# Optimization experiments

Hardware: AMD Instinct MI355X
Metric: run time of the kernel (lower is better)

## Reference

```python
import jax, jax.numpy as jnp
import numpy as np

B, S, D, H = 2, 2048, 1024, 16
HD = D // H  # head_dim = 64
SCALE = 1.0 / np.sqrt(np.float32(D))  # original divides by sqrt(d_keys) == sqrt(d_model)


def setup_inputs() -> dict:
    key = jax.random.key(0)
    ks = jax.random.split(key, 8)
    inp = {
        "query": jax.random.normal(ks[0], (B, S, D), jnp.float32),
        "key": jax.random.normal(ks[1], (B, S, D), jnp.float32),
        "value": jax.random.normal(ks[2], (B, S, D), jnp.float32),
        # nn.Linear weights stored as [out, in]; y = x @ W.T
        "Wq": jax.random.normal(ks[3], (D, D), jnp.float32) * 0.02,
        "Wk": jax.random.normal(ks[4], (D, D), jnp.float32) * 0.02,
        "Wv": jax.random.normal(ks[5], (D, D), jnp.float32) * 0.02,
        "Wo": jax.random.normal(ks[6], (D, D), jnp.float32) * 0.02,
        "bo": jax.random.normal(ks[7], (D,), jnp.float32) * 0.02,
    }
    return inp


def reference(query, key, value, Wq, Wk, Wv, Wo, bo):
    # projections (no bias)
    Q = jnp.einsum('bsd,ed->bse', query, Wq)
    K = jnp.einsum('bsd,ed->bse', key, Wk)
    V = jnp.einsum('bsd,ed->bse', value, Wv)
    # split heads -> [B, H, S, HD]
    Q = Q.reshape(B, S, H, HD).transpose(0, 2, 1, 3)
    K = K.reshape(B, S, H, HD).transpose(0, 2, 1, 3)
    V = V.reshape(B, S, H, HD).transpose(0, 2, 1, 3)
    # scores [B,H,S,S]; note: scaled by 1/sqrt(d_model), matching the source
    scores = jnp.einsum('bhqd,bhkd->bhqk', Q, K) * SCALE
    attn = jax.nn.softmax(scores, axis=-1)  # dropout_ratio=0 -> identity
    ctx = jnp.einsum('bhqk,bhkd->bhqd', attn, V)
    ctx = ctx.transpose(0, 2, 1, 3).reshape(B, S, D)
    return jnp.einsum('bsd,ed->bse', ctx, Wo) + bo
```

## Files before the change

kernel.cpp:

```cpp
#include <hip/hip_runtime.h>
#include <hip/hip_bf16.h>

#define B_  2
#define S_  2048
#define D_  1024
#define H_  16
#define HD_ 64
#define SCALE_ 0.03125f

typedef __bf16 bf16;
typedef __attribute__((ext_vector_type(8))) __bf16 bf16x8;
typedef __attribute__((ext_vector_type(8))) unsigned short u16x8;
typedef __attribute__((ext_vector_type(4))) __bf16 bf16x4;
typedef __attribute__((ext_vector_type(4))) float f32x4;

__device__ __forceinline__ void gload_lds16(const void* g, void* l) {
  __builtin_amdgcn_global_load_lds(
      (const __attribute__((address_space(1))) unsigned int*)g,
      (__attribute__((address_space(3))) unsigned int*)l,
      16, 0, 0);
}

__device__ __forceinline__ bf16x8 load8(const float* p) {
  const float4 a = *(const float4*)p;
  const float4 b = *(const float4*)(p + 4);
  bf16x8 r;
  r[0] = (bf16)a.x; r[1] = (bf16)a.y; r[2] = (bf16)a.z; r[3] = (bf16)a.w;
  r[4] = (bf16)b.x; r[5] = (bf16)b.y; r[6] = (bf16)b.z; r[7] = (bf16)b.w;
  return r;
}
__device__ __forceinline__ bf16x8 load8(const bf16* p) {
  return *(const bf16x8*)p;
}

__global__ __launch_bounds__(256)
void wconv_kernel(const float* __restrict__ Wq, const float* __restrict__ Wk,
                  const float* __restrict__ Wv, const float* __restrict__ Wo,
                  bf16* __restrict__ dst)
{
  const int n4  = (blockIdx.x * 256 + threadIdx.x) * 4;
  const int m   = n4 >> 20;
  const int off = n4 & ((1 << 20) - 1);
  const float* src = m == 0 ? Wq : (m == 1 ? Wk : (m == 2 ? Wv : Wo));
  const float4 a = *(const float4*)(src + off);
  bf16x4 o = {(bf16)a.x, (bf16)a.y, (bf16)a.z, (bf16)a.w};
  *(bf16x4*)(dst + n4) = o;
}

__global__ __launch_bounds__(256, 2)
void gemm_qkv_b_kernel(const float* __restrict__ Aq, const float* __restrict__ Ak,
                       const float* __restrict__ Av, const bf16* __restrict__ Wb,
                       bf16* __restrict__ Cq, bf16* __restrict__ Ck,
                       bf16* __restrict__ Cv)
{
  __shared__ bf16 lA[128 * 32];
  __shared__ bf16 lB[128 * 32];

  const int sel = blockIdx.y >> 3;
  const int bn  = blockIdx.y & 7;
  const float* A  = sel == 0 ? Aq : (sel == 1 ? Ak : Av);
  const bf16*  Bw = Wb + ((size_t)sel << 20);
  bf16*        C  = sel == 0 ? Cq : (sel == 1 ? Ck : Cv);
  const float scale = sel == 0 ? SCALE_ : 1.0f;

  const int t    = threadIdx.x;
  const int wave = t >> 6;
  const int lane = t & 63;
  const int quad = lane >> 4;
  const int l16  = lane & 15;
  const int bm = blockIdx.x;
  const int wm = (wave >> 1) * 64;
  const int wn = (wave & 1) * 64;

  const int srow = t >> 2;
  const int scol = (t & 3) * 8;
  const float* gA  = A  + (size_t)(bm * 128 + srow) * D_ + scol;
  const bf16*  gBb = Bw + (size_t)(bn * 128 + srow) * D_ + scol;

  f32x4 acc[4][4] = {};

  for (int k0 = 0; k0 < D_; k0 += 32) {
    const bf16x8 a0 = load8(gA);
    const bf16x8 a1 = load8(gA + (size_t)64 * D_);

    __syncthreads();
    *(bf16x8*)(lA + srow * 32 + scol)        = a0;
    *(bf16x8*)(lA + (srow + 64) * 32 + scol) = a1;
    gload_lds16(gBb,                   (char*)lB + wave * 1024);
    gload_lds16(gBb + (size_t)64 * D_, (char*)lB + 4096 + wave * 1024);
    __syncthreads();

    bf16x8 af[4], bfr[4];
#pragma unroll
    for (int i = 0; i < 4; ++i) {
      af[i]  = *(const bf16x8*)(lA + (wm + i * 16 + l16) * 32 + quad * 8);
      bfr[i] = *(const bf16x8*)(lB + (wn + i * 16 + l16) * 32 + quad * 8);
    }
#pragma unroll
    for (int mi = 0; mi < 4; ++mi)
#pragma unroll
      for (int ni = 0; ni < 4; ++ni)
        acc[mi][ni] = __builtin_amdgcn_mfma_f32_16x16x32_bf16(
            af[mi], bfr[ni], acc[mi][ni], 0, 0, 0);

    gA  += 32;
    gBb += 32;
  }

#pragma unroll
  for (int mi = 0; mi < 4; ++mi) {
#pragma unroll
    for (int ni = 0; ni < 4; ++ni) {
      const int col = bn * 128 + wn + ni * 16 + l16;
#pragma unroll
      for (int r = 0; r < 4; ++r) {
        const int row = bm * 128 + wm + mi * 16 + quad * 4 + r;
        C[(size_t)row * D_ + col] = (bf16)(acc[mi][ni][r] * scale);
      }
    }
  }
}

__global__ __launch_bounds__(256, 2)
void gemm_out_b_kernel(const bf16* __restrict__ A, const bf16* __restrict__ Bw,
                       const float* __restrict__ bias, float* __restrict__ C)
{
  __shared__ bf16 lA[128 * 32];
  __shared__ bf16 lB[64 * 32];

  const int t    = threadIdx.x;
  const int wave = t >> 6;
  const int lane = t & 63;
  const int quad = lane >> 4;
  const int l16  = lane & 15;
  const int bm = blockIdx.x;
  const int bn = blockIdx.y;
  const int wm = wave * 32;

  const int srow = t >> 2;
  const int scol = (t & 3) * 8;
  const bf16* gA = A  + (size_t)(bm * 128 + srow) * D_ + scol;
  const bf16* gB = Bw + (size_t)(bn * 64 + srow) * D_ + scol;

  f32x4 acc[2][4] = {};

  for (int k0 = 0; k0 < D_; k0 += 32) {
    __syncthreads();
    gload_lds16(gA,                   (char*)lA + wave * 1024);
    gload_lds16(gA + (size_t)64 * D_, (char*)lA + 4096 + wave * 1024);
    gload_lds16(gB,                   (char*)lB + wave * 1024);
    __syncthreads();

    bf16x8 af[2], bfr[4];
#pragma unroll
    for (int i = 0; i < 2; ++i)
      af[i]  = *(const bf16x8*)(lA + (wm + i * 16 + l16) * 32 + quad * 8);
#pragma unroll
    for (int i = 0; i < 4; ++i)
      bfr[i] = *(const bf16x8*)(lB + (i * 16 + l16) * 32 + quad * 8);
#pragma unroll
    for (int mi = 0; mi < 2; ++mi)
#pragma unroll
      for (int ni = 0; ni < 4; ++ni)
        acc[mi][ni] = __builtin_amdgcn_mfma_f32_16x16x32_bf16(
            af[mi], bfr[ni], acc[mi][ni], 0, 0, 0);

    gA += 32;
    gB += 32;
  }

  float bv[4];
#pragma unroll
  for (int ni = 0; ni < 4; ++ni)
    bv[ni] = bias[bn * 64 + ni * 16 + l16];
#pragma unroll
  for (int mi = 0; mi < 2; ++mi) {
#pragma unroll
    for (int ni = 0; ni < 4; ++ni) {
      const int col = bn * 64 + ni * 16 + l16;
#pragma unroll
      for (int r = 0; r < 4; ++r) {
        const int row = bm * 128 + wm + mi * 16 + quad * 4 + r;
        C[(size_t)row * D_ + col] = acc[mi][ni][r] + bv[ni];
      }
    }
  }
}

__global__ __launch_bounds__(256, 2)
void gemm_qkv_kernel(const float* __restrict__ Aq, const float* __restrict__ Ak,
                     const float* __restrict__ Av, const float* __restrict__ Wq,
                     const float* __restrict__ Wk, const float* __restrict__ Wv,
                     bf16* __restrict__ Cq, bf16* __restrict__ Ck,
                     bf16* __restrict__ Cv)
{
  __shared__ bf16 lA[128 * 32];
  __shared__ bf16 lB[128 * 32];

  const int sel = blockIdx.y >> 3;
  const int bn  = blockIdx.y & 7;
  const float* A  = sel == 0 ? Aq : (sel == 1 ? Ak : Av);
  const float* Bw = sel == 0 ? Wq : (sel == 1 ? Wk : Wv);
  bf16*        C  = sel == 0 ? Cq : (sel == 1 ? Ck : Cv);
  const float scale = sel == 0 ? SCALE_ : 1.0f;

  const int t    = threadIdx.x;
  const int wave = t >> 6;
  const int lane = t & 63;
  const int quad = lane >> 4;
  const int l16  = lane & 15;
  const int bm = blockIdx.x;
  const int wm = (wave >> 1) * 64;
  const int wn = (wave & 1) * 64;

  const int srow = t >> 2;
  const int scol = (t & 3) * 8;
  const float* gA = A  + (size_t)(bm * 128 + srow) * D_ + scol;
  const float* gB = Bw + (size_t)(bn * 128 + srow) * D_ + scol;

  f32x4 acc[4][4] = {};

  for (int k0 = 0; k0 < D_; k0 += 32) {
    const bf16x8 a0 = load8(gA);
    const bf16x8 a1 = load8(gA + (size_t)64 * D_);
    const bf16x8 b0 = load8(gB);
    const bf16x8 b1 = load8(gB + (size_t)64 * D_);

    __syncthreads();
    *(bf16x8*)(lA + srow * 32 + scol)        = a0;
    *(bf16x8*)(lA + (srow + 64) * 32 + scol) = a1;
    *(bf16x8*)(lB + srow * 32 + scol)        = b0;
    *(bf16x8*)(lB + (srow + 64) * 32 + scol) = b1;
    __syncthreads();

    bf16x8 af[4], bfr[4];
#pragma unroll
    for (int i = 0; i < 4; ++i) {
      af[i]  = *(const bf16x8*)(lA + (wm + i * 16 + l16) * 32 + quad * 8);
      bfr[i] = *(const bf16x8*)(lB + (wn + i * 16 + l16) * 32 + quad * 8);
    }
#pragma unroll
    for (int mi = 0; mi < 4; ++mi)
#pragma unroll
      for (int ni = 0; ni < 4; ++ni)
        acc[mi][ni] = __builtin_amdgcn_mfma_f32_16x16x32_bf16(
            af[mi], bfr[ni], acc[mi][ni], 0, 0, 0);

    gA += 32;
    gB += 32;
  }

#pragma unroll
  for (int mi = 0; mi < 4; ++mi) {
#pragma unroll
    for (int ni = 0; ni < 4; ++ni) {
      const int col = bn * 128 + wn + ni * 16 + l16;
#pragma unroll
      for (int r = 0; r < 4; ++r) {
        const int row = bm * 128 + wm + mi * 16 + quad * 4 + r;
        C[(size_t)row * D_ + col] = (bf16)(acc[mi][ni][r] * scale);
      }
    }
  }
}

__global__ __launch_bounds__(256, 2)
void gemm_out_kernel(const bf16* __restrict__ A, const float* __restrict__ Bw,
                     const float* __restrict__ bias, float* __restrict__ C)
{
  __shared__ bf16 lA[128 * 32];
  __shared__ bf16 lB[64 * 32];

  const int t    = threadIdx.x;
  const int wave = t >> 6;
  const int lane = t & 63;
  const int quad = lane >> 4;
  const int l16  = lane & 15;
  const int bm = blockIdx.x;
  const int bn = blockIdx.y;
  const int wm = wave * 32;

  const int srow = t >> 2;
  const int scol = (t & 3) * 8;
  const bf16*  gA = A  + (size_t)(bm * 128 + srow) * D_ + scol;
  const float* gB = Bw + (size_t)(bn * 64 + srow) * D_ + scol;

  f32x4 acc[2][4] = {};

  for (int k0 = 0; k0 < D_; k0 += 32) {
    const bf16x8 a0 = load8(gA);
    const bf16x8 a1 = load8(gA + (size_t)64 * D_);
    const bf16x8 b0 = load8(gB);

    __syncthreads();
    *(bf16x8*)(lA + srow * 32 + scol)        = a0;
    *(bf16x8*)(lA + (srow + 64) * 32 + scol) = a1;
    *(bf16x8*)(lB + srow * 32 + scol)        = b0;
    __syncthreads();

    bf16x8 af[2], bfr[4];
#pragma unroll
    for (int i = 0; i < 2; ++i)
      af[i]  = *(const bf16x8*)(lA + (wm + i * 16 + l16) * 32 + quad * 8);
#pragma unroll
    for (int i = 0; i < 4; ++i)
      bfr[i] = *(const bf16x8*)(lB + (i * 16 + l16) * 32 + quad * 8);
#pragma unroll
    for (int mi = 0; mi < 2; ++mi)
#pragma unroll
      for (int ni = 0; ni < 4; ++ni)
        acc[mi][ni] = __builtin_amdgcn_mfma_f32_16x16x32_bf16(
            af[mi], bfr[ni], acc[mi][ni], 0, 0, 0);

    gA += 32;
    gB += 32;
  }

  float bv[4];
#pragma unroll
  for (int ni = 0; ni < 4; ++ni)
    bv[ni] = bias[bn * 64 + ni * 16 + l16];
#pragma unroll
  for (int mi = 0; mi < 2; ++mi) {
#pragma unroll
    for (int ni = 0; ni < 4; ++ni) {
      const int col = bn * 64 + ni * 16 + l16;
#pragma unroll
      for (int r = 0; r < 4; ++r) {
        const int row = bm * 128 + wm + mi * 16 + quad * 4 + r;
        C[(size_t)row * D_ + col] = acc[mi][ni][r] + bv[ni];
      }
    }
  }
}

__global__ __launch_bounds__(256, 2)
void attn_kernel(const bf16* Q, const bf16* __restrict__ K,
                 const bf16* __restrict__ V, bf16* O)
{
  __shared__ bf16 lQ[64 * 72];
  __shared__ bf16 lK[64 * 72];
  __shared__ bf16 lVT[80 * 72];
  __shared__ bf16 lP[4][16 * 72];

  const int t    = threadIdx.x;
  const int wave = t >> 6;
  const int lane = t & 63;
  const int quad = lane >> 4;
  const int l16  = lane & 15;

  const int flat = blockIdx.y * 32 + blockIdx.x;
  const int qt   = (flat >> 3) & 31;
  const int bh   = (flat & 7) * 4 + (flat >> 8);
  const size_t headoff =
      (size_t)(bh >> 4) * ((size_t)S_ * D_) + (size_t)(bh & 15) * HD_;

  for (int i = t; i < 16 * 72; i += 256) {
    const int rr = i / 72, cc = i % 72;
    lVT[(64 + rr) * 72 + cc] = (bf16)((rr == 0 && cc < 64) ? 1.0f : 0.0f);
  }

  const int sr  = t >> 3;
  const int scx = (t & 7) * 8;
  {
    const bf16x8 q0 = *(const bf16x8*)(Q + headoff + (size_t)(qt * 64 + sr) * D_ + scx);
    const bf16x8 q1 = *(const bf16x8*)(Q + headoff + (size_t)(qt * 64 + sr + 32) * D_ + scx);
    *(bf16x8*)(lQ + sr * 72 + scx)        = q0;
    *(bf16x8*)(lQ + (sr + 32) * 72 + scx) = q1;
  }
  __syncthreads();

  bf16x8 qf[2];
  {
    const int row = wave * 16 + l16;
#pragma unroll
    for (int ks = 0; ks < 2; ++ks)
      qf[ks] = *(const bf16x8*)(lQ + row * 72 + (ks * 4 + quad) * 8);
  }

  f32x4 acco[4] = {};
  f32x4 acc4 = {};

  const int dp = t & 31;
  const int kg = t >> 5;

  bf16x8 pk0, pk1;
  unsigned int pv[8];
  {
    const bf16* kb = K + headoff + (size_t)(sr) * D_ + scx;
    pk0 = load8(kb);
    pk1 = load8(kb + (size_t)32 * D_);
    const bf16* vb = V + headoff + (size_t)(kg * 8) * D_ + 2 * dp;
#pragma unroll
    for (int j = 0; j < 8; ++j)
      pv[j] = *(const unsigned int*)(vb + (size_t)j * D_);
  }

  for (int kt = 0; kt < S_ / 64; ++kt) {
    __syncthreads();

    *(bf16x8*)(lK + sr * 72 + scx)        = pk0;
    *(bf16x8*)(lK + (sr + 32) * 72 + scx) = pk1;
    {
      u16x8 w0, w1;
#pragma unroll
      for (int j = 0; j < 8; ++j) {
        w0[j] = (unsigned short)(pv[j] & 0xffffu);
        w1[j] = (unsigned short)(pv[j] >> 16);
      }
      *(u16x8*)(lVT + (2 * dp) * 72 + kg * 8)     = w0;
      *(u16x8*)(lVT + (2 * dp + 1) * 72 + kg * 8) = w1;
    }
    __syncthreads();

    if (kt + 1 < S_ / 64) {
      const bf16* kb = K + headoff + (size_t)((kt + 1) * 64 + sr) * D_ + scx;
      pk0 = load8(kb);
      pk1 = load8(kb + (size_t)32 * D_);
      const bf16* vb = V + headoff + (size_t)((kt + 1) * 64 + kg * 8) * D_ + 2 * dp;
#pragma unroll
      for (int j = 0; j < 8; ++j)
        pv[j] = *(const unsigned int*)(vb + (size_t)j * D_);
    }

    f32x4 sc[4] = {};
#pragma unroll
    for (int nt = 0; nt < 4; ++nt) {
#pragma unroll
      for (int ks = 0; ks < 2; ++ks) {
        const int krow = nt * 16 + l16;
        const bf16x8 kf = *(const bf16x8*)(lK + krow * 72 + (ks * 4 + quad) * 8);
        sc[nt] = __builtin_amdgcn_mfma_f32_16x16x32_bf16(qf[ks], kf, sc[nt], 0, 0, 0);
      }
    }

    bf16* lPw = lP[wave];
#pragma unroll
    for (int nt = 0; nt < 4; ++nt) {
#pragma unroll
      for (int r = 0; r < 4; ++r) {
        const float p = __expf(sc[nt][r]);
        lPw[(quad * 4 + r) * 72 + nt * 16 + l16] = (bf16)p;
      }
    }

    bf16x8 pf[2];
#pragma unroll
    for (int ks = 0; ks < 2; ++ks)
      pf[ks] = *(const bf16x8*)(lPw + l16 * 72 + ks * 32 + quad * 8);
#pragma unroll
    for (int dt = 0; dt < 4; ++dt) {
#pragma unroll
      for (int ks = 0; ks < 2; ++ks) {
        const bf16x8 vf =
            *(const bf16x8*)(lVT + (dt * 16 + l16) * 72 + ks * 32 + quad * 8);
        acco[dt] = __builtin_amdgcn_mfma_f32_16x16x32_bf16(pf[ks], vf, acco[dt], 0, 0, 0);
      }
    }
#pragma unroll
    for (int ks = 0; ks < 2; ++ks) {
      const bf16x8 vf1 =
          *(const bf16x8*)(lVT + (64 + l16) * 72 + ks * 32 + quad * 8);
      acc4 = __builtin_amdgcn_mfma_f32_16x16x32_bf16(pf[ks], vf1, acc4, 0, 0, 0);
    }
  }

  float den[4];
#pragma unroll
  for (int r = 0; r < 4; ++r)
    den[r] = 1.f / __shfl(acc4[r], lane & 48);
#pragma unroll
  for (int dt = 0; dt < 4; ++dt) {
#pragma unroll
    for (int r = 0; r < 4; ++r) {
      const int row = qt * 64 + wave * 16 + quad * 4 + r;
      const int d   = dt * 16 + l16;
      O[headoff + (size_t)row * D_ + d] = (bf16)(acco[dt][r] * den[r]);
    }
  }
}

extern "C" void kernel_launch(void* const* d_in, const int* in_sizes, int n_in,
                              void* d_out, int out_size, void* d_ws, size_t ws_size,
                              hipStream_t stream)
{
  const float* q  = (const float*)d_in[0];
  const float* k  = (const float*)d_in[1];
  const float* v  = (const float*)d_in[2];
  const float* Wq = (const float*)d_in[3];
  const float* Wk = (const float*)d_in[4];
  const float* Wv = (const float*)d_in[5];
  const float* Wo = (const float*)d_in[6];
  const float* bo = (const float*)d_in[7];
  float* outf = (float*)d_out;
  bf16*  outs = (bf16*)d_out;
  bf16*  wsb  = (bf16*)d_ws;

  const size_t SD = (size_t)S_ * D_;
  const size_t MD = (size_t)B_ * S_ * D_;

  dim3 blk(256);
  dim3 gqkv(B_ * S_ / 128, 24);
  dim3 gattn(S_ / 64, B_ * H_);
  dim3 gout(B_ * S_ / 128, D_ / 64);

  bf16* Kp = outs;
  bf16* Vp = outs + MD;

  if (ws_size >= (size_t)16 << 20) {
    bf16* Wb = wsb;
    bf16* Qp = wsb + MD;

    wconv_kernel<<<4096, blk, 0, stream>>>(Wq, Wk, Wv, Wo, Wb);
    gemm_qkv_b_kernel<<<gqkv, blk, 0, stream>>>(q, k, v, Wb, Qp, Kp, Vp);
    attn_kernel<<<gattn, blk, 0, stream>>>(Qp, Kp, Vp, Qp);
    gemm_out_b_kernel<<<gout, blk, 0, stream>>>(Qp, Wb + 3 * ((size_t)1 << 20),
                                                bo, outf);
  } else {
    bf16* Qp = wsb;

    gemm_qkv_kernel<<<gqkv, blk, 0, stream>>>(q, k, v, Wq, Wk, Wv,
                                              Qp, Kp, Vp);
    attn_kernel<<<gattn, blk, 0, stream>>>(Qp, Kp, Vp, Qp);
    gemm_out_kernel<<<gout, blk, 0, stream>>>(Qp, Wo, bo, outf);
  }
}
```

Baseline: 234.8 us.

## Double attention query tile per block and fold log2e into Q scaling

Each attention block now processes 128 query rows instead of 64, with every wave handling two 16-row tiles. Each K and V fragment read from LDS therefore feeds two MFMAs, and the grid is halved. The softmax denominator is now a per-lane register sum reduced with shuffles, replacing the extra ones-row MFMA. The exponent uses exp2, with log2e folded into the Q projection scale. An added block-wide barrier per iteration and higher register and LDS use per block may lower occupancy.

```diff
diff --git a/kernel.cpp b/kernel.cpp
--- a/kernel.cpp
+++ b/kernel.cpp
@@ -7,6 +7,8 @@
 #define H_  16
 #define HD_ 64
 #define SCALE_ 0.03125f
+#define LOG2E_ 1.4426950408889634f
+#define QSCALE_ (SCALE_ * LOG2E_)
 
 typedef __bf16 bf16;
 typedef __attribute__((ext_vector_type(8))) __bf16 bf16x8;
@@ -61,7 +63,7 @@
   const float* A  = sel == 0 ? Aq : (sel == 1 ? Ak : Av);
   const bf16*  Bw = Wb + ((size_t)sel << 20);
   bf16*        C  = sel == 0 ? Cq : (sel == 1 ? Ck : Cv);
-  const float scale = sel == 0 ? SCALE_ : 1.0f;
+  const float scale = sel == 0 ? QSCALE_ : 1.0f;
 
   const int t    = threadIdx.x;
   const int wave = t >> 6;
@@ -202,7 +204,7 @@
   const float* A  = sel == 0 ? Aq : (sel == 1 ? Ak : Av);
   const float* Bw = sel == 0 ? Wq : (sel == 1 ? Wk : Wv);
   bf16*        C  = sel == 0 ? Cq : (sel == 1 ? Ck : Cv);
-  const float scale = sel == 0 ? SCALE_ : 1.0f;
+  const float scale = sel == 0 ? QSCALE_ : 1.0f;
 
   const int t    = threadIdx.x;
   const int wave = t >> 6;
@@ -338,10 +340,10 @@
 void attn_kernel(const bf16* Q, const bf16* __restrict__ K,
                  const bf16* __restrict__ V, bf16* O)
 {
-  __shared__ bf16 lQ[64 * 72];
+  __shared__ bf16 lQ[128 * 72];
   __shared__ bf16 lK[64 * 72];
-  __shared__ bf16 lVT[80 * 72];
-  __shared__ bf16 lP[4][16 * 72];
+  __shared__ bf16 lVT[64 * 72];
+  __shared__ bf16 lP[4][32 * 72];
 
   const int t    = threadIdx.x;
   const int wave = t >> 6;
@@ -349,37 +351,32 @@
   const int quad = lane >> 4;
   const int l16  = lane & 15;
 
-  const int flat = blockIdx.y * 32 + blockIdx.x;
-  const int qt   = (flat >> 3) & 31;
-  const int bh   = (flat & 7) * 4 + (flat >> 8);
+  const int flat = blockIdx.y * 16 + blockIdx.x;
+  const int qt   = (flat >> 3) & 15;
+  const int bh   = (flat & 7) * 4 + (flat >> 7);
   const size_t headoff =
       (size_t)(bh >> 4) * ((size_t)S_ * D_) + (size_t)(bh & 15) * HD_;
 
-  for (int i = t; i < 16 * 72; i += 256) {
-    const int rr = i / 72, cc = i % 72;
-    lVT[(64 + rr) * 72 + cc] = (bf16)((rr == 0 && cc < 64) ? 1.0f : 0.0f);
-  }
-
   const int sr  = t >> 3;
   const int scx = (t & 7) * 8;
-  {
-    const bf16x8 q0 = *(const bf16x8*)(Q + headoff + (size_t)(qt * 64 + sr) * D_ + scx);
-    const bf16x8 q1 = *(const bf16x8*)(Q + headoff + (size_t)(qt * 64 + sr + 32) * D_ + scx);
-    *(bf16x8*)(lQ + sr * 72 + scx)        = q0;
-    *(bf16x8*)(lQ + (sr + 32) * 72 + scx) = q1;
+#pragma unroll
+  for (int i = 0; i < 4; ++i) {
+    const bf16x8 qv =
+        *(const bf16x8*)(Q + headoff + (size_t)(qt * 128 + sr + 32 * i) * D_ + scx);
+    *(bf16x8*)(lQ + (sr + 32 * i) * 72 + scx) = qv;
   }
   __syncthreads();
 
-  bf16x8 qf[2];
-  {
-    const int row = wave * 16 + l16;
+  bf16x8 qf[2][2];
+#pragma unroll
+  for (int m = 0; m < 2; ++m)
 #pragma unroll
     for (int ks = 0; ks < 2; ++ks)
-      qf[ks] = *(const bf16x8*)(lQ + row * 72 + (ks * 4 + quad) * 8);
-  }
-
-  f32x4 acco[4] = {};
-  f32x4 acc4 = {};
+      qf[m][ks] = *(const bf16x8*)(lQ + (wave * 32 + m * 16 + l16) * 72 +
+                                   (ks * 4 + quad) * 8);
+
+  f32x4 acco[2][4] = {};
+  float den[2] = {0.f, 0.f};
 
   const int dp = t & 31;
   const int kg = t >> 5;
@@ -387,7 +384,7 @@
   bf16x8 pk0, pk1;
   unsigned int pv[8];
   {
-    const bf16* kb = K + headoff + (size_t)(sr) * D_ + scx;
+    const bf16* kb = K + headoff + (size_t)sr * D_ + scx;
     pk0 = load8(kb);
     pk1 = load8(kb + (size_t)32 * D_);
     const bf16* vb = V + headoff + (size_t)(kg * 8) * D_ + 2 * dp;
@@ -423,59 +420,74 @@
         pv[j] = *(const unsigned int*)(vb + (size_t)j * D_);
     }
 
-    f32x4 sc[4] = {};
+    f32x4 sc[2][4] = {};
 #pragma unroll
     for (int nt = 0; nt < 4; ++nt) {
 #pragma unroll
       for (int ks = 0; ks < 2; ++ks) {
-        const int krow = nt * 16 + l16;
-        const bf16x8 kf = *(const bf16x8*)(lK + krow * 72 + (ks * 4 + quad) * 8);
-        sc[nt] = __builtin_amdgcn_mfma_f32_16x16x32_bf16(qf[ks], kf, sc[nt], 0, 0, 0);
+        const bf16x8 kf =
+            *(const bf16x8*)(lK + (nt * 16 + l16) * 72 + (ks * 4 + quad) * 8);
+#pragma unroll
+        for (int m = 0; m < 2; ++m)
+          sc[m][nt] = __builtin_amdgcn_mfma_f32_16x16x32_bf16(
+              kf, qf[m][ks], sc[m][nt], 0, 0, 0);
       }
     }
 
     bf16* lPw = lP[wave];
 #pragma unroll
-    for (int nt = 0; nt < 4; ++nt) {
-#pragma unroll
-      for (int r = 0; r < 4; ++r) {
-        const float p = __expf(sc[nt][r]);
-        lPw[(quad * 4 + r) * 72 + nt * 16 + l16] = (bf16)p;
-      }
-    }
-
-    bf16x8 pf[2];
-#pragma unroll
-    for (int ks = 0; ks < 2; ++ks)
-      pf[ks] = *(const bf16x8*)(lPw + l16 * 72 + ks * 32 + quad * 8);
+    for (int m = 0; m < 2; ++m) {
+#pragma unroll
+      for (int nt = 0; nt < 4; ++nt) {
+        bf16x4 pw;
+#pragma unroll
+        for (int r = 0; r < 4; ++r) {
+          const float p = __builtin_amdgcn_exp2f(sc[m][nt][r]);
+          pw[r] = (bf16)p;
+          den[m] += p;
+        }
+        *(bf16x4*)(lPw + (m * 16 + l16) * 72 + nt * 16 + quad * 4) = pw;
+      }
+    }
+
+    __syncthreads();
+
+    bf16x8 pf[2][2];
+#pragma unroll
+    for (int m = 0; m < 2; ++m)
+#pragma unroll
+      for (int ks = 0; ks < 2; ++ks)
+        pf[m][ks] = *(const bf16x8*)(lPw + (m * 16 + l16) * 72 +
+                                     ks * 32 + quad * 8);
 #pragma unroll
     for (int dt = 0; dt < 4; ++dt) {
 #pragma unroll
       for (int ks = 0; ks < 2; ++ks) {
         const bf16x8 vf =
-            *(const bf16x8*)(lVT + (dt * 16 + l16) * 72 + ks * 32 + quad * 8);
-        acco[dt] = __builtin_amdgcn_mfma_f32_16x16x32_bf16(pf[ks], vf, acco[dt], 0, 0, 0);
-      }
-    }
-#pragma unroll
-    for (int ks = 0; ks < 2; ++ks) {
-      const bf16x8 vf1 =
-          *(const bf16x8*)(lVT + (64 + l16) * 72 + ks * 32 + quad * 8);
-      acc4 = __builtin_amdgcn_mfma_f32_16x16x32_bf16(pf[ks], vf1, acc4, 0, 0, 0);
-    }
-  }
-
-  float den[4];
-#pragma unroll
-  for (int r = 0; r < 4; ++r)
-    den[r] = 1.f / __shfl(acc4[r], lane & 48);
-#pragma unroll
-  for (int dt = 0; dt < 4; ++dt) {
+            *(const bf16x8*)(lVT + (dt * 16 + l16) * 72 + (ks * 4 + quad) * 8);
+#pragma unroll
+        for (int m = 0; m < 2; ++m)
+          acco[m][dt] = __builtin_amdgcn_mfma_f32_16x16x32_bf16(
+              pf[m][ks], vf, acco[m][dt], 0, 0, 0);
+      }
+    }
+  }
+
+#pragma unroll
+  for (int m = 0; m < 2; ++m) {
+    den[m] += __shfl_xor(den[m], 16);
+    den[m] += __shfl_xor(den[m], 32);
+  }
+#pragma unroll
+  for (int m = 0; m < 2; ++m) {
 #pragma unroll
     for (int r = 0; r < 4; ++r) {
-      const int row = qt * 64 + wave * 16 + quad * 4 + r;
-      const int d   = dt * 16 + l16;
-      O[headoff + (size_t)row * D_ + d] = (bf16)(acco[dt][r] * den[r]);
+      const float rd  = 1.f / __shfl(den[m], quad * 4 + r);
+      const int   row = qt * 128 + wave * 32 + m * 16 + quad * 4 + r;
+#pragma unroll
+      for (int dt = 0; dt < 4; ++dt)
+        O[headoff + (size_t)row * D_ + dt * 16 + l16] =
+            (bf16)(acco[m][dt][r] * rd);
     }
   }
 }
@@ -501,7 +513,7 @@
 
   dim3 blk(256);
   dim3 gqkv(B_ * S_ / 128, 24);
-  dim3 gattn(S_ / 64, B_ * H_);
+  dim3 gattn(S_ / 128, B_ * H_);
   dim3 gout(B_ * S_ / 128, D_ / 64);
 
   bf16* Kp = outs;
```

New measurement: 217.4 us. 7.4% less time.
